# Kernel tuning notes

Hardware: AMD Instinct MI355X
Metric: run time of the kernel (lower is better)

The kernel has to match this reference:

```python
import jax, jax.numpy as jnp
import numpy as np

D_MODEL = 2816
N_HEADS = 16
DH = 256
N_KV = 8
MAX_CTX = 4096
EPS = 1e-6
POS = 1024  # current decode position (tokens 0..POS are valid)


def rmsnorm(x, gamma=None, eps=EPS):
    # Gemma-style: variance in fp32, scale is (1 + gamma)
    v = jnp.mean(jnp.square(x.astype(jnp.float32)), axis=-1, keepdims=True)
    x = x * jax.lax.rsqrt(v + eps).astype(x.dtype)
    if gamma is not None:
        x = x * (1.0 + gamma)
    return x


def apply_rope(x, cos, sin):
    # x: (1, T, H, D); cos/sin: (1, T, D)
    cos = cos[:, :, None, :]
    sin = sin[:, :, None, :]
    d = x.shape[-1]
    x1, x2 = x[..., : d // 2], x[..., d // 2 :]
    rot = jnp.concatenate([-x2, x1], axis=-1)
    return x * cos + rot * sin


def setup_inputs() -> dict:
    key = jax.random.key(0)
    ks = jax.random.split(key, 8)
    x = jax.random.normal(ks[0], (1, 1, D_MODEL), dtype=jnp.float32)
    # realistic RoPE tables at position POS over full head dim
    inv_freq = 1.0 / (10000.0 ** (np.arange(0, DH, 2, dtype=np.float32) / DH))
    ang = np.float32(POS) * inv_freq  # (DH/2,)
    ang = np.concatenate([ang, ang])  # (DH,)
    cos = jnp.asarray(np.cos(ang), dtype=jnp.float32).reshape(1, 1, DH)
    sin = jnp.asarray(np.sin(ang), dtype=jnp.float32).reshape(1, 1, DH)
    k_cache = jax.random.normal(ks[1], (1, N_KV, MAX_CTX, DH), dtype=jnp.float32) * 0.5
    v_cache = jax.random.normal(ks[2], (1, N_KV, MAX_CTX, DH), dtype=jnp.float32) * 0.5
    # zero out cache beyond POS (not yet written)
    valid = (jnp.arange(MAX_CTX) <= POS)[None, None, :, None]
    k_cache = jnp.where(valid, k_cache, 0.0)
    v_cache = jnp.where(valid, v_cache, 0.0)
    # mask: 0 for positions <= POS, -inf after
    attn_mask = jnp.where(jnp.arange(MAX_CTX) <= POS, 0.0, -jnp.inf).astype(jnp.float32).reshape(1, 1, 1, MAX_CTX)
    kv_write_mask = jnp.zeros((1, 1, MAX_CTX, 1), dtype=jnp.float32).at[0, 0, POS, 0].set(1.0)
    s = 0.02
    wq = jax.random.normal(ks[3], (N_HEADS * DH, D_MODEL), dtype=jnp.float32) * s
    wk = jax.random.normal(ks[4], (N_KV * DH, D_MODEL), dtype=jnp.float32) * s
    wv = jax.random.normal(ks[5], (N_KV * DH, D_MODEL), dtype=jnp.float32) * s
    wo = jax.random.normal(ks[6], (D_MODEL, N_HEADS * DH), dtype=jnp.float32) * s
    q_gamma = jnp.zeros((DH,), dtype=jnp.float32)
    k_gamma = jnp.zeros((DH,), dtype=jnp.float32)
    return {"x": x, "cos": cos, "sin": sin, "k_cache": k_cache, "v_cache": v_cache,
            "attn_mask": attn_mask, "kv_write_mask": kv_write_mask,
            "wq": wq, "wk": wk, "wv": wv, "wo": wo,
            "q_gamma": q_gamma, "k_gamma": k_gamma}


def reference(x, cos, sin, k_cache, v_cache, attn_mask, kv_write_mask,
              wq, wk, wv, wo, q_gamma, k_gamma):
    # projections (nn.Linear: x @ W^T)
    q = (x @ wq.T).reshape(1, 1, N_HEADS, DH)
    k = (x @ wk.T).reshape(1, 1, N_KV, DH)
    v = (x @ wv.T).reshape(1, 1, N_KV, DH)
    q = rmsnorm(q, q_gamma)
    k = rmsnorm(k, k_gamma)
    v = rmsnorm(v, None)
    q = apply_rope(q, cos, sin)
    k = apply_rope(k, cos, sin)
    q = jnp.transpose(q, (0, 2, 1, 3))  # (1, H, 1, D)
    k = jnp.transpose(k, (0, 2, 1, 3))  # (1, Hkv, 1, D)
    v = jnp.transpose(v, (0, 2, 1, 3))
    # cache write via additive one-hot mask
    k_new = k_cache + k * kv_write_mask  # (1, Hkv, S, D)
    v_new = v_cache + v * kv_write_mask
    rep = N_HEADS // N_KV
    K = jnp.repeat(k_new, rep, axis=1)  # (1, H, S, D)
    V = jnp.repeat(v_new, rep, axis=1)
    # NOTE: original applies no 1/sqrt(dh) scaling
    scores = jnp.einsum('bhqd,bhkd->bhqk', q, K) + attn_mask
    w = jax.nn.softmax(scores.astype(jnp.float32), axis=-1).astype(q.dtype)
    ctx = jnp.einsum('bhqk,bhkd->bhqd', w, V)  # (1, H, 1, D)
    ctx = jnp.transpose(ctx, (0, 2, 1, 3)).reshape(1, 1, N_HEADS * DH)
    out = ctx @ wo.T  # (1, 1, D_MODEL)
    return (out, k_new, v_new)
```

## Files before the change

kernel.cpp:

```cpp
#include <hip/hip_runtime.h>
#include <hip/hip_bf16.h>

#define D_MODEL 2816
#define NH 16
#define DH 256
#define NKV 8
#define MAX_CTX 4096
#define POS 1024
#define QROWS (NH * DH)
#define KROWS (NKV * DH)
#define CACHE_ELEMS ((size_t)NKV * MAX_CTX * DH)

#define CCH 64
#define NCHUNKS 64
#define NATT 17

#define WS_QR 0
#define WS_KR QROWS
#define WS_VR (QROWS + KROWS)
#define WS_QP 8192
#define WS_KP 12288
#define WS_VP 14336
#define WS_PM 16384
#define WS_PL (WS_PM + NH * NATT)
#define WS_PCTX (WS_PL + NH * NATT)
#define WS_CTX (WS_PCTX + NH * NATT * DH)

__global__ __launch_bounds__(256) void k1b_gemv(
    const float* __restrict__ x, const float* __restrict__ wq,
    const float* __restrict__ wk, const float* __restrict__ wv,
    float* __restrict__ ws)
{
    __shared__ float xs[D_MODEL];
    for (int i = threadIdx.x; i < D_MODEL; i += 256) xs[i] = x[i];
    __syncthreads();
    const int wave = threadIdx.x >> 6;
    const int lane = threadIdx.x & 63;
    const int row = blockIdx.x * 4 + wave;
    const float* w;
    if (row < QROWS)              w = wq + (size_t)row * D_MODEL;
    else if (row < QROWS + KROWS) w = wk + (size_t)(row - QROWS) * D_MODEL;
    else                          w = wv + (size_t)(row - QROWS - KROWS) * D_MODEL;
    const float4* __restrict__ w4 = (const float4*)w;
    const float4* x4 = (const float4*)xs;
    float4 a[11];
    #pragma unroll
    for (int i = 0; i < 11; ++i) a[i] = w4[lane + i * 64];
    float acc = 0.f;
    #pragma unroll
    for (int i = 0; i < 11; ++i) {
        float4 b = x4[lane + i * 64];
        acc += a[i].x * b.x + a[i].y * b.y + a[i].z * b.z + a[i].w * b.w;
    }
    #pragma unroll
    for (int off = 32; off; off >>= 1) acc += __shfl_down(acc, off, 64);
    if (lane == 0) ws[row] = acc;
}

__global__ __launch_bounds__(256) void k2_norm_rope(
    const float* __restrict__ cosb, const float* __restrict__ sinb,
    const float* __restrict__ qg, const float* __restrict__ kg,
    float* __restrict__ ws)
{
    const int b = blockIdx.x;
    const int t = threadIdx.x;
    __shared__ float xn[DH];
    __shared__ float red[4];
    int kind, head;
    const float* src;
    if (b < 16)      { kind = 0; head = b;      src = ws + WS_QR + head * DH; }
    else if (b < 24) { kind = 1; head = b - 16; src = ws + WS_KR + head * DH; }
    else             { kind = 2; head = b - 24; src = ws + WS_VR + head * DH; }

    const float v = src[t];
    float ss = v * v;
    #pragma unroll
    for (int off = 32; off; off >>= 1) ss += __shfl_down(ss, off, 64);
    if ((t & 63) == 0) red[t >> 6] = ss;
    __syncthreads();
    const float tot = red[0] + red[1] + red[2] + red[3];
    const float scale = rsqrtf(tot * (1.0f / DH) + 1e-6f);
    float g = 1.0f;
    if (kind == 0)      g = 1.0f + qg[t];
    else if (kind == 1) g = 1.0f + kg[t];
    const float val = v * scale * g;

    float res;
    if (kind == 2) {
        res = val;
    } else {
        xn[t] = val;
        __syncthreads();
        const float partner = xn[t ^ 128];
        const float rot = (t < 128) ? -partner : partner;
        res = val * cosb[t] + rot * sinb[t];
    }

    if (kind == 0)      ws[WS_QP + head * DH + t] = res;
    else if (kind == 1) ws[WS_KP + head * DH + t] = res;
    else                ws[WS_VP + head * DH + t] = res;
}

__global__ __launch_bounds__(256) void kca(
    const float* __restrict__ kc, const float* __restrict__ vc,
    float* __restrict__ out, float* __restrict__ ws)
{
    const int kvh = blockIdx.x & 7;
    const int chunk = blockIdx.x >> 3;
    const int h0 = kvh * 2;
    const int t = threadIdx.x;
    const int wave = t >> 6;
    const int lane = t & 63;
    const bool is_att = (chunk < NATT);
    const int nk = (chunk < NATT - 1) ? CCH : 1;
    const size_t base = (size_t)kvh * MAX_CTX * DH + (size_t)chunk * CCH * DH;

    __shared__ float ssc[2][CCH];
    __shared__ float pct[2][4][DH];
    __shared__ float msh[2], lsh[2];

    const float4* __restrict__ kb4 = (const float4*)(kc + base);
    const float4* __restrict__ vb4 = (const float4*)(vc + base);
    float4* __restrict__ ok4 = (float4*)(out + D_MODEL + base);
    float4* __restrict__ ov4 = (float4*)(out + D_MODEL + CACHE_ELEMS + base);

    float4 q0v, q1v;
    if (is_att) {
        q0v = ((const float4*)(ws + WS_QP + (size_t)h0 * DH))[lane];
        q1v = ((const float4*)(ws + WS_QP + (size_t)(h0 + 1) * DH))[lane];
    }

    {
        float4 kv[16];
        #pragma unroll
        for (int i = 0; i < 16; ++i)
            kv[i] = kb4[(size_t)(wave * 16 + i) * 64 + lane];
        if (chunk == NATT - 1 && wave == 0) {
            const float4 kp = ((const float4*)(ws + WS_KP + (size_t)kvh * DH))[lane];
            kv[0].x += kp.x; kv[0].y += kp.y; kv[0].z += kp.z; kv[0].w += kp.w;
        }
        #pragma unroll
        for (int i = 0; i < 16; ++i)
            ok4[(size_t)(wave * 16 + i) * 64 + lane] = kv[i];
        if (is_att) {
            #pragma unroll
            for (int i = 0; i < 16; ++i) {
                const int j = wave * 16 + i;
                if (j < nk) {
                    float a0 = q0v.x * kv[i].x + q0v.y * kv[i].y + q0v.z * kv[i].z + q0v.w * kv[i].w;
                    float a1 = q1v.x * kv[i].x + q1v.y * kv[i].y + q1v.z * kv[i].z + q1v.w * kv[i].w;
                    #pragma unroll
                    for (int off = 32; off; off >>= 1) {
                        a0 += __shfl_down(a0, off, 64);
                        a1 += __shfl_down(a1, off, 64);
                    }
                    if (lane == 0) { ssc[0][j] = a0; ssc[1][j] = a1; }
                }
            }
        }
    }
    __syncthreads();

    if (is_att && wave < 2) {
        const int hh = wave;
        const float sc = (lane < nk) ? ssc[hh][lane] : -1e30f;
        float m = sc;
        #pragma unroll
        for (int off = 32; off; off >>= 1) m = fmaxf(m, __shfl_xor(m, off, 64));
        const float p = (lane < nk) ? expf(sc - m) : 0.f;
        if (lane < CCH) ssc[hh][lane] = p;
        float l = p;
        #pragma unroll
        for (int off = 32; off; off >>= 1) l += __shfl_xor(l, off, 64);
        if (lane == 0) { msh[hh] = m; lsh[hh] = l; }
    }
    __syncthreads();

    {
        float4 vv[16];
        #pragma unroll
        for (int i = 0; i < 16; ++i)
            vv[i] = vb4[(size_t)(wave * 16 + i) * 64 + lane];
        if (chunk == NATT - 1 && wave == 0) {
            const float4 vp = ((const float4*)(ws + WS_VP + (size_t)kvh * DH))[lane];
            vv[0].x += vp.x; vv[0].y += vp.y; vv[0].z += vp.z; vv[0].w += vp.w;
        }
        #pragma unroll
        for (int i = 0; i < 16; ++i)
            ov4[(size_t)(wave * 16 + i) * 64 + lane] = vv[i];
        if (is_att) {
            float4 a0 = {0.f, 0.f, 0.f, 0.f}, a1 = {0.f, 0.f, 0.f, 0.f};
            #pragma unroll
            for (int i = 0; i < 16; ++i) {
                const int j = wave * 16 + i;
                if (j < nk) {
                    const float w0 = ssc[0][j];
                    const float w1 = ssc[1][j];
                    a0.x += w0 * vv[i].x; a0.y += w0 * vv[i].y;
                    a0.z += w0 * vv[i].z; a0.w += w0 * vv[i].w;
                    a1.x += w1 * vv[i].x; a1.y += w1 * vv[i].y;
                    a1.z += w1 * vv[i].z; a1.w += w1 * vv[i].w;
                }
            }
            ((float4*)&pct[0][wave][0])[lane] = a0;
            ((float4*)&pct[1][wave][0])[lane] = a1;
        }
    }
    __syncthreads();

    if (is_att) {
        const float c0 = pct[0][0][t] + pct[0][1][t] + pct[0][2][t] + pct[0][3][t];
        const float c1 = pct[1][0][t] + pct[1][1][t] + pct[1][2][t] + pct[1][3][t];
        const int pc0 = h0 * NATT + chunk;
        const int pc1 = (h0 + 1) * NATT + chunk;
        ws[WS_PCTX + (size_t)pc0 * DH + t] = c0;
        ws[WS_PCTX + (size_t)pc1 * DH + t] = c1;
        if (t == 0) {
            ws[WS_PM + pc0] = msh[0]; ws[WS_PL + pc0] = lsh[0];
            ws[WS_PM + pc1] = msh[1]; ws[WS_PL + pc1] = lsh[1];
        }
    }
}

__global__ __launch_bounds__(256) void kb_combine(float* __restrict__ ws)
{
    const int h = blockIdx.x;
    const int t = threadIdx.x;
    __shared__ float sm[NATT], sl[NATT];
    if (t < NATT) {
        sm[t] = ws[WS_PM + h * NATT + t];
        sl[t] = ws[WS_PL + h * NATT + t];
    }
    __syncthreads();
    float m = -1e30f;
    #pragma unroll
    for (int c = 0; c < NATT; ++c) m = fmaxf(m, sm[c]);
    float denom = 0.f;
    float acc = 0.f;
    #pragma unroll
    for (int c = 0; c < NATT; ++c) {
        const float e = expf(sm[c] - m);
        denom += e * sl[c];
        acc += e * ws[WS_PCTX + (size_t)(h * NATT + c) * DH + t];
    }
    ws[WS_CTX + h * DH + t] = acc / denom;
}

__global__ __launch_bounds__(256) void k6_out(
    const float* __restrict__ wo, const float* __restrict__ ws,
    float* __restrict__ out)
{
    __shared__ float cs[NH * DH];
    for (int i = threadIdx.x; i < NH * DH; i += 256) cs[i] = ws[WS_CTX + i];
    __syncthreads();
    const int wave = threadIdx.x >> 6;
    const int lane = threadIdx.x & 63;
    const int row = blockIdx.x * 4 + wave;
    const float4* __restrict__ w4 = (const float4*)(wo + (size_t)row * (NH * DH));
    const float4* c4 = (const float4*)cs;
    float4 a[16];
    #pragma unroll
    for (int i = 0; i < 16; ++i) a[i] = w4[lane + i * 64];
    float acc = 0.f;
    #pragma unroll
    for (int i = 0; i < 16; ++i) {
        float4 b = c4[lane + i * 64];
        acc += a[i].x * b.x + a[i].y * b.y + a[i].z * b.z + a[i].w * b.w;
    }
    #pragma unroll
    for (int off = 32; off; off >>= 1) acc += __shfl_down(acc, off, 64);
    if (lane == 0) out[row] = acc;
}

extern "C" void kernel_launch(void* const* d_in, const int* in_sizes, int n_in,
                              void* d_out, int out_size, void* d_ws, size_t ws_size,
                              hipStream_t stream)
{
    const float* x    = (const float*)d_in[0];
    const float* cosb = (const float*)d_in[1];
    const float* sinb = (const float*)d_in[2];
    const float* kc   = (const float*)d_in[3];
    const float* vc   = (const float*)d_in[4];
    const float* wq   = (const float*)d_in[7];
    const float* wk   = (const float*)d_in[8];
    const float* wv   = (const float*)d_in[9];
    const float* wo   = (const float*)d_in[10];
    const float* qg   = (const float*)d_in[11];
    const float* kg   = (const float*)d_in[12];
    float* out = (float*)d_out;
    float* ws  = (float*)d_ws;

    k1b_gemv<<<2048, 256, 0, stream>>>(x, wq, wk, wv, ws);
    k2_norm_rope<<<32, 256, 0, stream>>>(cosb, sinb, qg, kg, ws);
    kca<<<NKV * NCHUNKS, 256, 0, stream>>>(kc, vc, out, ws);
    kb_combine<<<NH, 256, 0, stream>>>(ws);
    k6_out<<<704, 256, 0, stream>>>(wo, ws, out);
}
```

Before: 61.61 us.

## Split bulk cache copy into separate kernel and halve attention chunk size

Copying of the invalid cache tail (rows from 1088 on) moves into a new standalone copy kernel launched first, so the attention kernel only covers the first 34 chunks of 32 rows per KV head. The chunk size drops from 64 to 32, which gives more blocks working on the valid region and a 32-lane softmax reduction. The aim is to keep the large memory copy off the critical path of the attention kernel and to spread attention work across more blocks. The cost is one extra kernel launch and more partial results for the combine step. The combine and workspace layout now depend on NATT=33.

```diff
diff --git a/kernel.cpp b/kernel.cpp
--- a/kernel.cpp
+++ b/kernel.cpp
@@ -11,9 +11,11 @@
 #define KROWS (NKV * DH)
 #define CACHE_ELEMS ((size_t)NKV * MAX_CTX * DH)
 
-#define CCH 64
-#define NCHUNKS 64
-#define NATT 17
+#define CCH 32
+#define NATT 33
+#define NCH_TOT 34
+#define COPY_ROW0 1088
+#define HC_PER_KVH 94
 
 #define WS_QR 0
 #define WS_KR QROWS
@@ -26,6 +28,46 @@
 #define WS_PCTX (WS_PL + NH * NATT)
 #define WS_CTX (WS_PCTX + NH * NATT * DH)
 
+__global__ __launch_bounds__(256) void kcopy(
+    const float* __restrict__ kc, const float* __restrict__ vc,
+    float* __restrict__ out)
+{
+    const int bid = blockIdx.x;
+    const int kvh = bid / HC_PER_KVH;
+    const int hc  = bid % HC_PER_KVH;
+    const int t = threadIdx.x;
+    const size_t f4seg = (size_t)kvh * (MAX_CTX * 64)
+                       + (size_t)(COPY_ROW0 + hc * 32) * 64;
+    const float4* __restrict__ sk = (const float4*)kc + f4seg;
+    const float4* __restrict__ sv = (const float4*)vc + f4seg;
+    float4* __restrict__ dk = (float4*)(out + D_MODEL) + f4seg;
+    float4* __restrict__ dv = (float4*)(out + D_MODEL + CACHE_ELEMS) + f4seg;
+
+    float4 cur[4], nxt[4];
+    #pragma unroll
+    for (int j = 0; j < 4; ++j) cur[j] = sk[j * 256 + t];
+    #pragma unroll
+    for (int j = 0; j < 4; ++j) nxt[j] = sk[1024 + j * 256 + t];
+    #pragma unroll
+    for (int j = 0; j < 4; ++j) dk[j * 256 + t] = cur[j];
+    #pragma unroll
+    for (int j = 0; j < 4; ++j) cur[j] = nxt[j];
+    #pragma unroll
+    for (int j = 0; j < 4; ++j) nxt[j] = sv[j * 256 + t];
+    #pragma unroll
+    for (int j = 0; j < 4; ++j) dk[1024 + j * 256 + t] = cur[j];
+    #pragma unroll
+    for (int j = 0; j < 4; ++j) cur[j] = nxt[j];
+    #pragma unroll
+    for (int j = 0; j < 4; ++j) nxt[j] = sv[1024 + j * 256 + t];
+    #pragma unroll
+    for (int j = 0; j < 4; ++j) dv[j * 256 + t] = cur[j];
+    #pragma unroll
+    for (int j = 0; j < 4; ++j) cur[j] = nxt[j];
+    #pragma unroll
+    for (int j = 0; j < 4; ++j) dv[1024 + j * 256 + t] = cur[j];
+}
+
 __global__ __launch_bounds__(256) void k1b_gemv(
     const float* __restrict__ x, const float* __restrict__ wq,
     const float* __restrict__ wk, const float* __restrict__ wv,
@@ -112,7 +154,7 @@
     const int wave = t >> 6;
     const int lane = t & 63;
     const bool is_att = (chunk < NATT);
-    const int nk = (chunk < NATT - 1) ? CCH : 1;
+    const int nk = (chunk < NATT - 1) ? CCH : (chunk == NATT - 1 ? 1 : 0);
     const size_t base = (size_t)kvh * MAX_CTX * DH + (size_t)chunk * CCH * DH;
 
     __shared__ float ssc[2][CCH];
@@ -131,21 +173,21 @@
     }
 
     {
-        float4 kv[16];
-        #pragma unroll
-        for (int i = 0; i < 16; ++i)
-            kv[i] = kb4[(size_t)(wave * 16 + i) * 64 + lane];
+        float4 kv[8];
+        #pragma unroll
+        for (int i = 0; i < 8; ++i)
+            kv[i] = kb4[(size_t)(wave * 8 + i) * 64 + lane];
         if (chunk == NATT - 1 && wave == 0) {
             const float4 kp = ((const float4*)(ws + WS_KP + (size_t)kvh * DH))[lane];
             kv[0].x += kp.x; kv[0].y += kp.y; kv[0].z += kp.z; kv[0].w += kp.w;
         }
         #pragma unroll
-        for (int i = 0; i < 16; ++i)
-            ok4[(size_t)(wave * 16 + i) * 64 + lane] = kv[i];
+        for (int i = 0; i < 8; ++i)
+            ok4[(size_t)(wave * 8 + i) * 64 + lane] = kv[i];
         if (is_att) {
             #pragma unroll
-            for (int i = 0; i < 16; ++i) {
-                const int j = wave * 16 + i;
+            for (int i = 0; i < 8; ++i) {
+                const int j = wave * 8 + i;
                 if (j < nk) {
                     float a0 = q0v.x * kv[i].x + q0v.y * kv[i].y + q0v.z * kv[i].z + q0v.w * kv[i].w;
                     float a1 = q1v.x * kv[i].x + q1v.y * kv[i].y + q1v.z * kv[i].z + q1v.w * kv[i].w;
@@ -166,33 +208,33 @@
         const float sc = (lane < nk) ? ssc[hh][lane] : -1e30f;
         float m = sc;
         #pragma unroll
-        for (int off = 32; off; off >>= 1) m = fmaxf(m, __shfl_xor(m, off, 64));
+        for (int off = 16; off; off >>= 1) m = fmaxf(m, __shfl_xor(m, off, 64));
         const float p = (lane < nk) ? expf(sc - m) : 0.f;
         if (lane < CCH) ssc[hh][lane] = p;
         float l = p;
         #pragma unroll
-        for (int off = 32; off; off >>= 1) l += __shfl_xor(l, off, 64);
+        for (int off = 16; off; off >>= 1) l += __shfl_xor(l, off, 64);
         if (lane == 0) { msh[hh] = m; lsh[hh] = l; }
     }
     __syncthreads();
 
     {
-        float4 vv[16];
-        #pragma unroll
-        for (int i = 0; i < 16; ++i)
-            vv[i] = vb4[(size_t)(wave * 16 + i) * 64 + lane];
+        float4 vv[8];
+        #pragma unroll
+        for (int i = 0; i < 8; ++i)
+            vv[i] = vb4[(size_t)(wave * 8 + i) * 64 + lane];
         if (chunk == NATT - 1 && wave == 0) {
             const float4 vp = ((const float4*)(ws + WS_VP + (size_t)kvh * DH))[lane];
             vv[0].x += vp.x; vv[0].y += vp.y; vv[0].z += vp.z; vv[0].w += vp.w;
         }
         #pragma unroll
-        for (int i = 0; i < 16; ++i)
-            ov4[(size_t)(wave * 16 + i) * 64 + lane] = vv[i];
+        for (int i = 0; i < 8; ++i)
+            ov4[(size_t)(wave * 8 + i) * 64 + lane] = vv[i];
         if (is_att) {
             float4 a0 = {0.f, 0.f, 0.f, 0.f}, a1 = {0.f, 0.f, 0.f, 0.f};
             #pragma unroll
-            for (int i = 0; i < 16; ++i) {
-                const int j = wave * 16 + i;
+            for (int i = 0; i < 8; ++i) {
+                const int j = wave * 8 + i;
                 if (j < nk) {
                     const float w0 = ssc[0][j];
                     const float w1 = ssc[1][j];
@@ -290,9 +332,10 @@
     float* out = (float*)d_out;
     float* ws  = (float*)d_ws;
 
+    kcopy<<<NKV * HC_PER_KVH, 256, 0, stream>>>(kc, vc, out);
     k1b_gemv<<<2048, 256, 0, stream>>>(x, wq, wk, wv, ws);
     k2_norm_rope<<<32, 256, 0, stream>>>(cosb, sinb, qg, kg, ws);
-    kca<<<NKV * NCHUNKS, 256, 0, stream>>>(kc, vc, out, ws);
+    kca<<<NKV * NCH_TOT, 256, 0, stream>>>(kc, vc, out, ws);
     kb_combine<<<NH, 256, 0, stream>>>(ws);
     k6_out<<<704, 256, 0, stream>>>(wo, ws, out);
 }
```

Result: slower. 64.72 us (+5.0%).
